# Optimization experiments

Hardware: AMD Instinct MI355X
Metric: run time of the kernel (lower is better)

The kernel has to match this reference:

```python
import jax, jax.numpy as jnp
import numpy as np

N = 50000          # nodes
E = 600000         # edges
D = 128            # g_dim = h1_dim = h2_dim
R = 8              # 2 * n_speakers**2, n_speakers=2
B = 10             # num_bases


def setup_inputs() -> dict:
    key = jax.random.key(0)
    ks = jax.random.split(key, 10)
    s = 1.0 / np.sqrt(D)
    return {
        "node_features": jax.random.normal(ks[0], (N, D), jnp.float32),
        "edge_index": jax.random.randint(ks[1], (2, E), 0, N, jnp.int64),
        "edge_type": jax.random.randint(ks[2], (E,), 0, R, jnp.int64),
        # RGCNConv params (basis decomposition)
        "basis": jax.random.normal(ks[3], (B, D, D), jnp.float32) * s,
        "comp": jax.random.normal(ks[4], (R, B), jnp.float32) * (1.0 / np.sqrt(B)),
        "root": jax.random.normal(ks[5], (D, D), jnp.float32) * s,
        "bias1": jnp.zeros((D,), jnp.float32),
        # GraphConv params
        "w_rel": jax.random.normal(ks[6], (D, D), jnp.float32) * s,
        "b_rel": jnp.zeros((D,), jnp.float32),
        "w_root": jax.random.normal(ks[7], (D, D), jnp.float32) * s,
    }


def reference(node_features, edge_index, edge_type, basis, comp, root, bias1, w_rel, b_rel, w_root):
    x = node_features
    n = x.shape[0]
    r = comp.shape[0]
    src, dst = edge_index[0], edge_index[1]

    # ---- RGCNConv (basis decomposition, per-relation mean aggregation) ----
    # project through bases once: [N, B, D]
    xb = jnp.einsum('ni,bio->nbo', x, basis)
    # per-edge message: combine bases with relation coefficients  [E, D]
    msg = jnp.einsum('eb,ebo->eo', comp[edge_type], xb[src])
    # per-(dst, relation) mean normalization
    seg = dst * r + edge_type                       # [E]
    cnt = jax.ops.segment_sum(jnp.ones((msg.shape[0],), x.dtype), seg, num_segments=n * r)
    norm = 1.0 / jnp.maximum(cnt[seg], 1.0)         # [E]
    agg = jax.ops.segment_sum(msg * norm[:, None], dst, num_segments=n)  # [N, D]
    h1 = agg + x @ root + bias1

    # ---- GraphConv (add aggregation of neighbors + root transform) ----
    nbr = jax.ops.segment_sum(h1[src], dst, num_segments=n)  # [N, D]
    out = nbr @ w_rel.T + b_rel + h1 @ w_root.T
    return out
```

## Files before the change

### kernel.cpp

```cpp
#include <hip/hip_runtime.h>
#include <stdint.h>

#define N_NODES 50000
#define E_EDGES 600000
#define D 128
#define R_REL 8
#define B_BASES 10
#define RN (R_REL * N_NODES)

typedef __attribute__((ext_vector_type(8))) short bf16x8;
typedef __attribute__((ext_vector_type(4))) float f32x4;

__device__ __forceinline__ short f2b(float f) {
    uint32_t u = __float_as_uint(f);
    u += 0x7fff + ((u >> 16) & 1);
    return (short)(u >> 16);
}
__device__ __forceinline__ float b2f(uint16_t u) {
    return __uint_as_float((uint32_t)u << 16);
}

__device__ __forceinline__ void lds_barrier() {
    __builtin_amdgcn_sched_barrier(0);
    asm volatile("s_waitcnt lgkmcnt(0)\n\ts_barrier" ::: "memory");
    __builtin_amdgcn_sched_barrier(0);
}

__global__ __launch_bounds__(256) void k_front(const float* __restrict__ x,
                                               unsigned short* __restrict__ xb,
                                               const int* __restrict__ dst,
                                               const int* __restrict__ et,
                                               int* __restrict__ cntr,
                                               const float* __restrict__ basis,
                                               const float* __restrict__ comp,
                                               const float* __restrict__ root,
                                               const float* __restrict__ wrel,
                                               const float* __restrict__ wroot,
                                               short* __restrict__ wt,
                                               short* __restrict__ wrel_b,
                                               short* __restrict__ wroot_b) {
    const int XB_N = N_NODES * D / 8;
    int tid = blockIdx.x * 256 + threadIdx.x;
    if (tid < XB_N) {
        const float4* s = (const float4*)x + (size_t)tid * 2;
        float4 v0 = s[0], v1 = s[1];
        union { uint4 u; unsigned short h[8]; } pk;
        pk.h[0] = (unsigned short)f2b(v0.x); pk.h[1] = (unsigned short)f2b(v0.y);
        pk.h[2] = (unsigned short)f2b(v0.z); pk.h[3] = (unsigned short)f2b(v0.w);
        pk.h[4] = (unsigned short)f2b(v1.x); pk.h[5] = (unsigned short)f2b(v1.y);
        pk.h[6] = (unsigned short)f2b(v1.z); pk.h[7] = (unsigned short)f2b(v1.w);
        ((uint4*)xb)[tid] = pk.u;
    } else if (tid < XB_N + E_EDGES) {
        int e = tid - XB_N;
        atomicAdd(&cntr[dst[e] * R_REL + et[e]], 1);
    } else {
        int t2 = tid - XB_N - E_EDGES;
        if (t2 < 9 * D * D) {
            int s = t2 >> 14;
            int rem = t2 & 16383;
            int j = rem >> 7, i = rem & 127;
            float v;
            if (s < 8) {
                v = 0.f;
#pragma unroll
                for (int b = 0; b < B_BASES; b++)
                    v += comp[s * B_BASES + b] * basis[b * D * D + i * D + j];
            } else {
                v = root[i * D + j];
            }
            wt[t2] = f2b(v);
        } else {
            int t3 = t2 - 9 * D * D;
            if (t3 < D * D) {
                wrel_b[t3]  = f2b(wrel[t3]);
                wroot_b[t3] = f2b(wroot[t3]);
            }
        }
    }
}

__device__ __forceinline__ int wave_scan_incl(int v) {
    int lane = threadIdx.x & 63;
#pragma unroll
    for (int off = 1; off < 64; off <<= 1) {
        int n = __shfl_up(v, off, 64);
        if (lane >= off) v += n;
    }
    return v;
}

__global__ __launch_bounds__(1024) void k_scan_a(const int* __restrict__ in,
                                                 int* __restrict__ out,
                                                 int* __restrict__ bsum, int n) {
    __shared__ int wsum[16];
    int t = threadIdx.x, lane = t & 63, wid = t >> 6;
    int g = blockIdx.x * 1024 + t;
    int v = (g < n) ? in[g] : 0;
    int isc = wave_scan_incl(v);
    if (lane == 63) wsum[wid] = isc;
    __syncthreads();
    if (wid == 0) {
        int wv = (lane < 16) ? wsum[lane] : 0;
        int wsc = wave_scan_incl(wv);
        if (lane < 16) wsum[lane] = wsc - wv;
    }
    __syncthreads();
    if (g < n) out[g] = wsum[wid] + isc - v;
    if (t == 1023 && bsum) bsum[blockIdx.x] = wsum[15] + isc;
}

__global__ __launch_bounds__(1024) void k_scan_c(int* __restrict__ out,
                                                 const int* __restrict__ bsum, int n) {
    int g = blockIdx.x * 1024 + threadIdx.x;
    if (g < n) out[g] += bsum[blockIdx.x];
}

__global__ __launch_bounds__(256) void k_bucket(const int* __restrict__ src,
                                                const int* __restrict__ dst,
                                                const int* __restrict__ et,
                                                int* __restrict__ seg_off,
                                                int* __restrict__ es1) {
    int e = blockIdx.x * 256 + threadIdx.x;
    if (e >= E_EDGES) return;
    int key = dst[e] * R_REL + et[e];
    int pos = atomicAdd(&seg_off[key], 1);
    es1[pos] = src[e];
}

__global__ __launch_bounds__(256) void k_aggmean(const unsigned short* __restrict__ xb,
                                                 const int* __restrict__ es1,
                                                 const int* __restrict__ seg_off,
                                                 unsigned short* __restrict__ mx) {
    int t = threadIdx.x;
    int sw = t >> 4, l = t & 15;
    int k = blockIdx.x * 16 + sw;
    if (k >= RN) return;
    int start = (k == 0) ? 0 : seg_off[k - 1];
    int end = seg_off[k];
    size_t loff = (size_t)l * 8;

    if (end - start == 1) {
        uint4 v0 = *(const uint4*)(xb + (size_t)es1[start] * D + loff);
        *(uint4*)(mx + (size_t)k * D + loff) = v0;
        return;
    }

    float ax[8];
#pragma unroll
    for (int q = 0; q < 8; q++) ax[q] = 0.f;
    int pos = start;
    for (; pos + 2 <= end; pos += 2) {
        int s0 = es1[pos], s1 = es1[pos + 1];
        uint4 v0 = *(const uint4*)(xb + (size_t)s0 * D + loff);
        uint4 v1 = *(const uint4*)(xb + (size_t)s1 * D + loff);
        const uint32_t* w0 = (const uint32_t*)&v0;
        const uint32_t* w1 = (const uint32_t*)&v1;
#pragma unroll
        for (int q = 0; q < 4; q++) {
            ax[q * 2]     += b2f((uint16_t)w0[q]) + b2f((uint16_t)w1[q]);
            ax[q * 2 + 1] += b2f((uint16_t)(w0[q] >> 16)) + b2f((uint16_t)(w1[q] >> 16));
        }
    }
    if (pos < end) {
        int s0 = es1[pos];
        uint4 v0 = *(const uint4*)(xb + (size_t)s0 * D + loff);
        const uint32_t* w0 = (const uint32_t*)&v0;
#pragma unroll
        for (int q = 0; q < 4; q++) {
            ax[q * 2]     += b2f((uint16_t)w0[q]);
            ax[q * 2 + 1] += b2f((uint16_t)(w0[q] >> 16));
        }
    }
    float nm = (end > start) ? 1.f / (float)(end - start) : 0.f;
    union { uint4 u; unsigned short h[8]; } pk;
#pragma unroll
    for (int q = 0; q < 8; q++) pk.h[q] = (unsigned short)f2b(ax[q] * nm);
    *(uint4*)(mx + (size_t)k * D + loff) = pk.u;
}

__global__ __launch_bounds__(256) void k_h1_gemm(const unsigned short* __restrict__ mx,
                                                 const unsigned short* __restrict__ xb,
                                                 const short* __restrict__ wt,
                                                 const float* __restrict__ bias1,
                                                 unsigned short* __restrict__ h1b) {
    __shared__ short ws[2][128 * 128];
    int t = threadIdx.x;
    int wave = t >> 6, lane = t & 63, quad = lane >> 4, l16 = lane & 15;
    int base = blockIdx.x * 128;
    int n0 = base + wave * 32 + l16;
    int n1 = n0 + 16;
    int nc0 = n0 < N_NODES ? n0 : N_NODES - 1;
    int nc1 = n1 < N_NODES ? n1 : N_NODES - 1;
    int ci0 = wave * 8;

    auto aptr = [&](int nc, int s) -> const unsigned short* {
        return (s < 8) ? mx + ((size_t)nc * 8 + s) * D : xb + (size_t)nc * D;
    };

    uint4 aReg[2][2][4];
    {
        uint4 b0[8];
#pragma unroll
        for (int i = 0; i < 8; i++) {
            int row = (ci0 + i) * 4 + quad;
            b0[i] = *(const uint4*)(wt + row * D + (l16 << 3));
        }
#pragma unroll
        for (int kc = 0; kc < 4; kc++) {
            int co = (kc * 4 + quad) * 8;
            aReg[0][0][kc] = *(const uint4*)(aptr(nc0, 0) + co);
            aReg[0][1][kc] = *(const uint4*)(aptr(nc1, 0) + co);
            aReg[1][0][kc] = *(const uint4*)(aptr(nc0, 1) + co);
            aReg[1][1][kc] = *(const uint4*)(aptr(nc1, 1) + co);
        }
#pragma unroll
        for (int i = 0; i < 8; i++) {
            int row = (ci0 + i) * 4 + quad;
            *(uint4*)&ws[0][row * 128 + ((l16 ^ (row & 15)) << 3)] = b0[i];
        }
    }
    lds_barrier();

    f32x4 acc[2][8];
#pragma unroll
    for (int tl = 0; tl < 2; tl++)
#pragma unroll
        for (int jt = 0; jt < 8; jt++) acc[tl][jt] = (f32x4){0.f, 0.f, 0.f, 0.f};

    for (int s = 0; s < 9; s++) {
        int cur = s & 1;
        uint4 bn[8];
        if (s + 1 < 9) {
            const short* wb = wt + (size_t)(s + 1) * D * D;
#pragma unroll
            for (int i = 0; i < 8; i++) {
                int row = (ci0 + i) * 4 + quad;
                bn[i] = *(const uint4*)(wb + row * D + (l16 << 3));
            }
        }
#pragma unroll
        for (int kc = 0; kc < 4; kc++) {
            int c0 = kc * 4 + quad;
            bf16x8 a0 = *(bf16x8*)&aReg[cur][0][kc];
            bf16x8 a1 = *(bf16x8*)&aReg[cur][1][kc];
#pragma unroll
            for (int jt = 0; jt < 8; jt++) {
                bf16x8 b = *(const bf16x8*)&ws[cur][(jt * 16 + l16) * 128 + ((c0 ^ l16) << 3)];
                acc[0][jt] = __builtin_amdgcn_mfma_f32_16x16x32_bf16(a0, b, acc[0][jt], 0, 0, 0);
                acc[1][jt] = __builtin_amdgcn_mfma_f32_16x16x32_bf16(a1, b, acc[1][jt], 0, 0, 0);
            }
        }
        if (s + 2 <= 8) {
#pragma unroll
            for (int kc = 0; kc < 4; kc++) {
                int co = (kc * 4 + quad) * 8;
                aReg[cur][0][kc] = *(const uint4*)(aptr(nc0, s + 2) + co);
                aReg[cur][1][kc] = *(const uint4*)(aptr(nc1, s + 2) + co);
            }
        }
        if (s + 1 < 9) {
#pragma unroll
            for (int i = 0; i < 8; i++) {
                int row = (ci0 + i) * 4 + quad;
                *(uint4*)&ws[cur ^ 1][row * 128 + ((l16 ^ (row & 15)) << 3)] = bn[i];
            }
        }
        lds_barrier();
    }

#pragma unroll
    for (int tl = 0; tl < 2; tl++) {
#pragma unroll
        for (int reg = 0; reg < 4; reg++) {
            int node = base + wave * 32 + tl * 16 + quad * 4 + reg;
            if (node >= N_NODES) continue;
#pragma unroll
            for (int jt = 0; jt < 8; jt++) {
                int col = jt * 16 + l16;
                float v = acc[tl][jt][reg] + bias1[col];
                h1b[(size_t)node * D + col] = (unsigned short)f2b(v);
            }
        }
    }
}

__global__ __launch_bounds__(256) void k_agg_nbr(const unsigned short* __restrict__ h1b,
                                                 const int* __restrict__ es1,
                                                 const int* __restrict__ seg_off,
                                                 unsigned short* __restrict__ nbr) {
    int t = threadIdx.x;
    int wave = t >> 6, lane = t & 63, sub = lane >> 4, l = lane & 15;
    int d = blockIdx.x * 16 + wave * 4 + sub;
    if (d >= N_NODES) return;
    int start = (d == 0) ? 0 : seg_off[d * R_REL - 1];
    int end = seg_off[d * R_REL + 7];
    float acc[8];
#pragma unroll
    for (int j = 0; j < 8; j++) acc[j] = 0.f;
    size_t loff = (size_t)l * 8;

    int pos = start;
    for (; pos + 4 <= end; pos += 4) {
        int i0 = es1[pos], i1 = es1[pos + 1], i2 = es1[pos + 2], i3 = es1[pos + 3];
        uint4 v0 = *(const uint4*)(h1b + (size_t)i0 * D + loff);
        uint4 v1 = *(const uint4*)(h1b + (size_t)i1 * D + loff);
        uint4 v2 = *(const uint4*)(h1b + (size_t)i2 * D + loff);
        uint4 v3 = *(const uint4*)(h1b + (size_t)i3 * D + loff);
        const uint32_t* w0 = (const uint32_t*)&v0;
        const uint32_t* w1 = (const uint32_t*)&v1;
        const uint32_t* w2 = (const uint32_t*)&v2;
        const uint32_t* w3 = (const uint32_t*)&v3;
#pragma unroll
        for (int q = 0; q < 4; q++) {
            acc[q * 2]     += b2f((uint16_t)w0[q]) + b2f((uint16_t)w1[q]) +
                              b2f((uint16_t)w2[q]) + b2f((uint16_t)w3[q]);
            acc[q * 2 + 1] += b2f((uint16_t)(w0[q] >> 16)) + b2f((uint16_t)(w1[q] >> 16)) +
                              b2f((uint16_t)(w2[q] >> 16)) + b2f((uint16_t)(w3[q] >> 16));
        }
    }
    for (; pos < end; pos++) {
        int i0 = es1[pos];
        uint4 v0 = *(const uint4*)(h1b + (size_t)i0 * D + loff);
        const uint32_t* w0 = (const uint32_t*)&v0;
#pragma unroll
        for (int q = 0; q < 4; q++) {
            acc[q * 2]     += b2f((uint16_t)w0[q]);
            acc[q * 2 + 1] += b2f((uint16_t)(w0[q] >> 16));
        }
    }

    union { uint4 u; unsigned short h[8]; } pk;
#pragma unroll
    for (int j = 0; j < 8; j++) pk.h[j] = (unsigned short)f2b(acc[j]);
    *(uint4*)(nbr + (size_t)d * D + loff) = pk.u;
}

__global__ __launch_bounds__(256) void k_out2(const unsigned short* __restrict__ h1b,
                                              const unsigned short* __restrict__ nbr,
                                              const short* __restrict__ wroot_b,
                                              const short* __restrict__ wrel_b,
                                              const float* __restrict__ brel,
                                              float* __restrict__ out) {
    __shared__ short ws[2][128 * 128];
    int t = threadIdx.x;
    int wave = t >> 6, lane = t & 63, quad = lane >> 4, l16 = lane & 15;
    int base = blockIdx.x * 128;
    int n0 = base + wave * 32 + l16;
    int n1 = n0 + 16;
    int nc0 = n0 < N_NODES ? n0 : N_NODES - 1;
    int nc1 = n1 < N_NODES ? n1 : N_NODES - 1;
    int ci0 = wave * 8;

    uint4 aReg[2][2][4];
    {
        uint4 b0[8];
#pragma unroll
        for (int i = 0; i < 8; i++) {
            int row = (ci0 + i) * 4 + quad;
            b0[i] = *(const uint4*)(wroot_b + row * D + (l16 << 3));
        }
#pragma unroll
        for (int kc = 0; kc < 4; kc++) {
            int co = (kc * 4 + quad) * 8;
            aReg[0][0][kc] = *(const uint4*)(h1b + (size_t)nc0 * D + co);
            aReg[0][1][kc] = *(const uint4*)(h1b + (size_t)nc1 * D + co);
            aReg[1][0][kc] = *(const uint4*)(nbr + (size_t)nc0 * D + co);
            aReg[1][1][kc] = *(const uint4*)(nbr + (size_t)nc1 * D + co);
        }
#pragma unroll
        for (int i = 0; i < 8; i++) {
            int row = (ci0 + i) * 4 + quad;
            *(uint4*)&ws[0][row * 128 + ((l16 ^ (row & 15)) << 3)] = b0[i];
        }
    }
    lds_barrier();

    f32x4 acc[2][8];
#pragma unroll
    for (int tl = 0; tl < 2; tl++)
#pragma unroll
        for (int jt = 0; jt < 8; jt++) acc[tl][jt] = (f32x4){0.f, 0.f, 0.f, 0.f};

#pragma unroll
    for (int s = 0; s < 2; s++) {
        int cur = s & 1;
        uint4 bn[8];
        if (s == 0) {
#pragma unroll
            for (int i = 0; i < 8; i++) {
                int row = (ci0 + i) * 4 + quad;
                bn[i] = *(const uint4*)(wrel_b + row * D + (l16 << 3));
            }
        }
#pragma unroll
        for (int kc = 0; kc < 4; kc++) {
            int c0 = kc * 4 + quad;
            bf16x8 a0 = *(bf16x8*)&aReg[cur][0][kc];
            bf16x8 a1 = *(bf16x8*)&aReg[cur][1][kc];
#pragma unroll
            for (int jt = 0; jt < 8; jt++) {
                bf16x8 b = *(const bf16x8*)&ws[cur][(jt * 16 + l16) * 128 + ((c0 ^ l16) << 3)];
                acc[0][jt] = __builtin_amdgcn_mfma_f32_16x16x32_bf16(a0, b, acc[0][jt], 0, 0, 0);
                acc[1][jt] = __builtin_amdgcn_mfma_f32_16x16x32_bf16(a1, b, acc[1][jt], 0, 0, 0);
            }
        }
        if (s == 0) {
#pragma unroll
            for (int i = 0; i < 8; i++) {
                int row = (ci0 + i) * 4 + quad;
                *(uint4*)&ws[1][row * 128 + ((l16 ^ (row & 15)) << 3)] = bn[i];
            }
            lds_barrier();
        }
    }

#pragma unroll
    for (int tl = 0; tl < 2; tl++) {
#pragma unroll
        for (int reg = 0; reg < 4; reg++) {
            int node = base + wave * 32 + tl * 16 + quad * 4 + reg;
            if (node >= N_NODES) continue;
#pragma unroll
            for (int jt = 0; jt < 8; jt++) {
                int col = jt * 16 + l16;
                out[(size_t)node * D + col] = acc[tl][jt][reg] + brel[col];
            }
        }
    }
}

extern "C" void kernel_launch(void* const* d_in, const int* in_sizes, int n_in,
                              void* d_out, int out_size, void* d_ws, size_t ws_size,
                              hipStream_t stream) {
    const float* x     = (const float*)d_in[0];
    const int*   ei    = (const int*)d_in[1];
    const int*   et    = (const int*)d_in[2];
    const float* basis = (const float*)d_in[3];
    const float* comp  = (const float*)d_in[4];
    const float* root  = (const float*)d_in[5];
    const float* bias1 = (const float*)d_in[6];
    const float* wrel  = (const float*)d_in[7];
    const float* brel  = (const float*)d_in[8];
    const float* wroot = (const float*)d_in[9];
    float* out = (float*)d_out;
    const int* src = ei;
    const int* dst = ei + E_EDGES;

    char* p = (char*)d_ws;
    auto alloc = [&](size_t bytes) { char* q = p; p += (bytes + 255) & ~(size_t)255; return q; };
    short* wt      = (short*)alloc((size_t)9 * D * D * sizeof(short));
    short* wrel_b  = (short*)alloc(D * D * sizeof(short));
    short* wroot_b = (short*)alloc(D * D * sizeof(short));
    int*   cntr    = (int*)alloc((size_t)RN * sizeof(int));
    int*   seg_off = (int*)alloc((size_t)RN * sizeof(int));
    int*   es1     = (int*)alloc((size_t)(E_EDGES + 16) * sizeof(int));
    int*   bsum    = (int*)alloc(1024 * sizeof(int));
    unsigned short* xb  = (unsigned short*)alloc((size_t)N_NODES * D * sizeof(unsigned short));
    unsigned short* mx  = (unsigned short*)alloc((size_t)RN * D * sizeof(unsigned short));
    unsigned short* h1b = (unsigned short*)alloc((size_t)N_NODES * D * sizeof(unsigned short));
    unsigned short* nbr = xb;

    hipMemsetAsync(cntr, 0, (size_t)RN * sizeof(int), stream);

    const int XB_N = N_NODES * D / 8;
    int nfront = (XB_N + E_EDGES + 9 * D * D + D * D + 255) / 256;
    k_front<<<nfront, 256, 0, stream>>>(x, xb, dst, et, cntr,
                                        basis, comp, root, wrel, wroot,
                                        wt, wrel_b, wroot_b);

    int nscan = (RN + 1023) / 1024;
    k_scan_a<<<nscan, 1024, 0, stream>>>(cntr, seg_off, bsum, RN);
    k_scan_a<<<1, 1024, 0, stream>>>(bsum, bsum, nullptr, nscan);
    k_scan_c<<<nscan, 1024, 0, stream>>>(seg_off, bsum, RN);

    k_bucket<<<(E_EDGES + 255) / 256, 256, 0, stream>>>(src, dst, et, seg_off, es1);

    k_aggmean<<<RN / 16, 256, 0, stream>>>(xb, es1, seg_off, mx);

    int nb2 = (N_NODES + 127) / 128;
    int na = (N_NODES + 15) / 16;
    k_h1_gemm<<<nb2, 256, 0, stream>>>(mx, xb, wt, bias1, h1b);
    k_agg_nbr<<<na, 256, 0, stream>>>(h1b, es1, seg_off, nbr);
    k_out2<<<nb2, 256, 0, stream>>>(h1b, nbr, wroot_b, wrel_b, brel, out);
}
```

Before: 268.9 us.

## Reorder RGCN to transform-then-gather, removing per-relation mean buffer

```diff
diff --git a/kernel.cpp b/kernel.cpp
--- a/kernel.cpp
+++ b/kernel.cpp
@@ -127,62 +127,9 @@
     es1[pos] = src[e];
 }
 
-__global__ __launch_bounds__(256) void k_aggmean(const unsigned short* __restrict__ xb,
-                                                 const int* __restrict__ es1,
-                                                 const int* __restrict__ seg_off,
-                                                 unsigned short* __restrict__ mx) {
-    int t = threadIdx.x;
-    int sw = t >> 4, l = t & 15;
-    int k = blockIdx.x * 16 + sw;
-    if (k >= RN) return;
-    int start = (k == 0) ? 0 : seg_off[k - 1];
-    int end = seg_off[k];
-    size_t loff = (size_t)l * 8;
-
-    if (end - start == 1) {
-        uint4 v0 = *(const uint4*)(xb + (size_t)es1[start] * D + loff);
-        *(uint4*)(mx + (size_t)k * D + loff) = v0;
-        return;
-    }
-
-    float ax[8];
-#pragma unroll
-    for (int q = 0; q < 8; q++) ax[q] = 0.f;
-    int pos = start;
-    for (; pos + 2 <= end; pos += 2) {
-        int s0 = es1[pos], s1 = es1[pos + 1];
-        uint4 v0 = *(const uint4*)(xb + (size_t)s0 * D + loff);
-        uint4 v1 = *(const uint4*)(xb + (size_t)s1 * D + loff);
-        const uint32_t* w0 = (const uint32_t*)&v0;
-        const uint32_t* w1 = (const uint32_t*)&v1;
-#pragma unroll
-        for (int q = 0; q < 4; q++) {
-            ax[q * 2]     += b2f((uint16_t)w0[q]) + b2f((uint16_t)w1[q]);
-            ax[q * 2 + 1] += b2f((uint16_t)(w0[q] >> 16)) + b2f((uint16_t)(w1[q] >> 16));
-        }
-    }
-    if (pos < end) {
-        int s0 = es1[pos];
-        uint4 v0 = *(const uint4*)(xb + (size_t)s0 * D + loff);
-        const uint32_t* w0 = (const uint32_t*)&v0;
-#pragma unroll
-        for (int q = 0; q < 4; q++) {
-            ax[q * 2]     += b2f((uint16_t)w0[q]);
-            ax[q * 2 + 1] += b2f((uint16_t)(w0[q] >> 16));
-        }
-    }
-    float nm = (end > start) ? 1.f / (float)(end - start) : 0.f;
-    union { uint4 u; unsigned short h[8]; } pk;
-#pragma unroll
-    for (int q = 0; q < 8; q++) pk.h[q] = (unsigned short)f2b(ax[q] * nm);
-    *(uint4*)(mx + (size_t)k * D + loff) = pk.u;
-}
-
-__global__ __launch_bounds__(256) void k_h1_gemm(const unsigned short* __restrict__ mx,
-                                                 const unsigned short* __restrict__ xb,
+__global__ __launch_bounds__(256) void k_xw_gemm(const unsigned short* __restrict__ xb,
                                                  const short* __restrict__ wt,
-                                                 const float* __restrict__ bias1,
-                                                 unsigned short* __restrict__ h1b) {
+                                                 unsigned short* __restrict__ xw) {
     __shared__ short ws[2][128 * 128];
     int t = threadIdx.x;
     int wave = t >> 6, lane = t & 63, quad = lane >> 4, l16 = lane & 15;
@@ -193,11 +140,13 @@
     int nc1 = n1 < N_NODES ? n1 : N_NODES - 1;
     int ci0 = wave * 8;
 
-    auto aptr = [&](int nc, int s) -> const unsigned short* {
-        return (s < 8) ? mx + ((size_t)nc * 8 + s) * D : xb + (size_t)nc * D;
-    };
-
-    uint4 aReg[2][2][4];
+    uint4 aA[2][4];
+#pragma unroll
+    for (int kc = 0; kc < 4; kc++) {
+        int co = (kc * 4 + quad) * 8;
+        aA[0][kc] = *(const uint4*)(xb + (size_t)nc0 * D + co);
+        aA[1][kc] = *(const uint4*)(xb + (size_t)nc1 * D + co);
+    }
     {
         uint4 b0[8];
 #pragma unroll
@@ -206,26 +155,12 @@
             b0[i] = *(const uint4*)(wt + row * D + (l16 << 3));
         }
 #pragma unroll
-        for (int kc = 0; kc < 4; kc++) {
-            int co = (kc * 4 + quad) * 8;
-            aReg[0][0][kc] = *(const uint4*)(aptr(nc0, 0) + co);
-            aReg[0][1][kc] = *(const uint4*)(aptr(nc1, 0) + co);
-            aReg[1][0][kc] = *(const uint4*)(aptr(nc0, 1) + co);
-            aReg[1][1][kc] = *(const uint4*)(aptr(nc1, 1) + co);
-        }
-#pragma unroll
         for (int i = 0; i < 8; i++) {
             int row = (ci0 + i) * 4 + quad;
             *(uint4*)&ws[0][row * 128 + ((l16 ^ (row & 15)) << 3)] = b0[i];
         }
     }
     lds_barrier();
-
-    f32x4 acc[2][8];
-#pragma unroll
-    for (int tl = 0; tl < 2; tl++)
-#pragma unroll
-        for (int jt = 0; jt < 8; jt++) acc[tl][jt] = (f32x4){0.f, 0.f, 0.f, 0.f};
 
     for (int s = 0; s < 9; s++) {
         int cur = s & 1;
@@ -238,11 +173,16 @@
                 bn[i] = *(const uint4*)(wb + row * D + (l16 << 3));
             }
         }
+        f32x4 acc[2][8];
+#pragma unroll
+        for (int tl = 0; tl < 2; tl++)
+#pragma unroll
+            for (int jt = 0; jt < 8; jt++) acc[tl][jt] = (f32x4){0.f, 0.f, 0.f, 0.f};
 #pragma unroll
         for (int kc = 0; kc < 4; kc++) {
             int c0 = kc * 4 + quad;
-            bf16x8 a0 = *(bf16x8*)&aReg[cur][0][kc];
-            bf16x8 a1 = *(bf16x8*)&aReg[cur][1][kc];
+            bf16x8 a0 = *(bf16x8*)&aA[0][kc];
+            bf16x8 a1 = *(bf16x8*)&aA[1][kc];
 #pragma unroll
             for (int jt = 0; jt < 8; jt++) {
                 bf16x8 b = *(const bf16x8*)&ws[cur][(jt * 16 + l16) * 128 + ((c0 ^ l16) << 3)];
@@ -250,12 +190,18 @@
                 acc[1][jt] = __builtin_amdgcn_mfma_f32_16x16x32_bf16(a1, b, acc[1][jt], 0, 0, 0);
             }
         }
-        if (s + 2 <= 8) {
-#pragma unroll
-            for (int kc = 0; kc < 4; kc++) {
-                int co = (kc * 4 + quad) * 8;
-                aReg[cur][0][kc] = *(const uint4*)(aptr(nc0, s + 2) + co);
-                aReg[cur][1][kc] = *(const uint4*)(aptr(nc1, s + 2) + co);
+        unsigned short* xs = xw + (size_t)s * N_NODES * D;
+#pragma unroll
+        for (int tl = 0; tl < 2; tl++) {
+#pragma unroll
+            for (int reg = 0; reg < 4; reg++) {
+                int node = base + wave * 32 + tl * 16 + quad * 4 + reg;
+                if (node >= N_NODES) continue;
+#pragma unroll
+                for (int jt = 0; jt < 8; jt++) {
+                    int col = jt * 16 + l16;
+                    xs[(size_t)node * D + col] = (unsigned short)f2b(acc[tl][jt][reg]);
+                }
             }
         }
         if (s + 1 < 9) {
@@ -267,21 +213,70 @@
         }
         lds_barrier();
     }
-
-#pragma unroll
-    for (int tl = 0; tl < 2; tl++) {
-#pragma unroll
-        for (int reg = 0; reg < 4; reg++) {
-            int node = base + wave * 32 + tl * 16 + quad * 4 + reg;
-            if (node >= N_NODES) continue;
-#pragma unroll
-            for (int jt = 0; jt < 8; jt++) {
-                int col = jt * 16 + l16;
-                float v = acc[tl][jt][reg] + bias1[col];
-                h1b[(size_t)node * D + col] = (unsigned short)f2b(v);
-            }
-        }
-    }
+}
+
+__global__ __launch_bounds__(256) void k_h1_gather(const unsigned short* __restrict__ xw,
+                                                   const int* __restrict__ es1,
+                                                   const int* __restrict__ seg_off,
+                                                   const float* __restrict__ bias1,
+                                                   unsigned short* __restrict__ h1b) {
+    int t = threadIdx.x;
+    int wave = t >> 6, lane = t & 63, sub = lane >> 4, l = lane & 15;
+    int d = blockIdx.x * 16 + wave * 4 + sub;
+    if (d >= N_NODES) return;
+    size_t loff = (size_t)l * 8;
+
+    float h[8];
+    {
+        uint4 v0 = *(const uint4*)(xw + ((size_t)8 * N_NODES + d) * D + loff);
+        const uint32_t* w0 = (const uint32_t*)&v0;
+#pragma unroll
+        for (int q = 0; q < 4; q++) {
+            h[q * 2]     = b2f((uint16_t)w0[q])         + bias1[l * 8 + q * 2];
+            h[q * 2 + 1] = b2f((uint16_t)(w0[q] >> 16)) + bias1[l * 8 + q * 2 + 1];
+        }
+    }
+
+    int b_prev = (d == 0) ? 0 : seg_off[d * R_REL - 1];
+    for (int r = 0; r < R_REL; r++) {
+        int b_end = seg_off[d * R_REL + r];
+        if (b_end > b_prev) {
+            const unsigned short* xs = xw + (size_t)r * N_NODES * D;
+            float a[8];
+#pragma unroll
+            for (int q = 0; q < 8; q++) a[q] = 0.f;
+            int pos = b_prev;
+            for (; pos + 2 <= b_end; pos += 2) {
+                uint4 v0 = *(const uint4*)(xs + (size_t)es1[pos] * D + loff);
+                uint4 v1 = *(const uint4*)(xs + (size_t)es1[pos + 1] * D + loff);
+                const uint32_t* w0 = (const uint32_t*)&v0;
+                const uint32_t* w1 = (const uint32_t*)&v1;
+#pragma unroll
+                for (int q = 0; q < 4; q++) {
+                    a[q * 2]     += b2f((uint16_t)w0[q]) + b2f((uint16_t)w1[q]);
+                    a[q * 2 + 1] += b2f((uint16_t)(w0[q] >> 16)) + b2f((uint16_t)(w1[q] >> 16));
+                }
+            }
+            if (pos < b_end) {
+                uint4 v0 = *(const uint4*)(xs + (size_t)es1[pos] * D + loff);
+                const uint32_t* w0 = (const uint32_t*)&v0;
+#pragma unroll
+                for (int q = 0; q < 4; q++) {
+                    a[q * 2]     += b2f((uint16_t)w0[q]);
+                    a[q * 2 + 1] += b2f((uint16_t)(w0[q] >> 16));
+                }
+            }
+            float nm = 1.f / (float)(b_end - b_prev);
+#pragma unroll
+            for (int q = 0; q < 8; q++) h[q] += a[q] * nm;
+        }
+        b_prev = b_end;
+    }
+
+    union { uint4 u; unsigned short hh[8]; } pk;
+#pragma unroll
+    for (int q = 0; q < 8; q++) pk.hh[q] = (unsigned short)f2b(h[q]);
+    *(uint4*)(h1b + (size_t)d * D + loff) = pk.u;
 }
 
 __global__ __launch_bounds__(256) void k_agg_nbr(const unsigned short* __restrict__ h1b,
@@ -456,7 +451,7 @@
     int*   es1     = (int*)alloc((size_t)(E_EDGES + 16) * sizeof(int));
     int*   bsum    = (int*)alloc(1024 * sizeof(int));
     unsigned short* xb  = (unsigned short*)alloc((size_t)N_NODES * D * sizeof(unsigned short));
-    unsigned short* mx  = (unsigned short*)alloc((size_t)RN * D * sizeof(unsigned short));
+    unsigned short* xw  = (unsigned short*)alloc((size_t)9 * N_NODES * D * sizeof(unsigned short));
     unsigned short* h1b = (unsigned short*)alloc((size_t)N_NODES * D * sizeof(unsigned short));
     unsigned short* nbr = xb;
 
@@ -475,11 +470,10 @@
 
     k_bucket<<<(E_EDGES + 255) / 256, 256, 0, stream>>>(src, dst, et, seg_off, es1);
 
-    k_aggmean<<<RN / 16, 256, 0, stream>>>(xb, es1, seg_off, mx);
-
     int nb2 = (N_NODES + 127) / 128;
     int na = (N_NODES + 15) / 16;
-    k_h1_gemm<<<nb2, 256, 0, stream>>>(mx, xb, wt, bias1, h1b);
+    k_xw_gemm<<<nb2, 256, 0, stream>>>(xb, wt, xw);
+    k_h1_gather<<<na, 256, 0, stream>>>(xw, es1, seg_off, bias1, h1b);
     k_agg_nbr<<<na, 256, 0, stream>>>(h1b, es1, seg_off, nbr);
     k_out2<<<nb2, 256, 0, stream>>>(h1b, nbr, wroot_b, wrel_b, brel, out);
 }
```

Result: no change. 265.1 us (-1.4%).
